# Kernel tuning notes

Hardware: AMD Instinct MI355X
Metric: run time of the kernel (lower is better)

Reference implementation:

```python
import jax, jax.numpy as jnp
import numpy as np

N = 50000   # nodes
E = 800000  # edges (avg degree 16)
C = 64      # in_channels == out_channels


def _linear_params(key, fan_in, fan_out):
    kw, kb = jax.random.split(key)
    s = 1.0 / np.sqrt(fan_in)
    W = jax.random.uniform(kw, (fan_out, fan_in), minval=-s, maxval=s, dtype=jnp.float32)
    b = jax.random.uniform(kb, (fan_out,), minval=-s, maxval=s, dtype=jnp.float32)
    return W, b


def setup_inputs() -> dict:
    key = jax.random.key(0)
    ks = jax.random.split(key, 12)
    scalar = jax.random.normal(ks[0], (N, C), dtype=jnp.float32)
    vector = jax.random.normal(ks[1], (N, 3, C), dtype=jnp.float32)
    position = jax.random.normal(ks[2], (N, 3), dtype=jnp.float32)
    edge_index = jax.random.randint(ks[3], (2, E), 0, N, dtype=jnp.int64)
    edge_attr = jax.random.uniform(ks[4], (E,), dtype=jnp.float32)
    # Scalar_Conv params
    Wss, bss = _linear_params(ks[5], 2 * C, C)   # s_to_s
    Wvs, bvs = _linear_params(ks[6], 2 * C, C)   # v_to_s
    Wsl, bsl = _linear_params(ks[7], 2 * C, C)   # scalar_linear
    # Vector_Conv params
    Wsv, bsv = _linear_params(ks[8], 2 * C, C)   # s_to_v
    Wvv, bvv = _linear_params(ks[9], 2 * C, C)   # v_to_v
    Wvl, bvl = _linear_params(ks[10], 2 * C, C)  # vector_linear
    return dict(scalar=scalar, vector=vector, position=position,
                edge_index=edge_index, edge_attr=edge_attr,
                Wss=Wss, bss=bss, Wvs=Wvs, bvs=bvs, Wsl=Wsl, bsl=bsl,
                Wsv=Wsv, bsv=bsv, Wvv=Wvv, bvv=bvv, Wvl=Wvl, bvl=bvl)


def _norm(edge_index, edge_attr, num_nodes):
    # B=True path: edge_attr-weighted symmetric degree normalization
    row, col = edge_index[0], edge_index[1]
    deg = jax.ops.segment_sum(edge_attr, col, num_segments=num_nodes)
    deg_safe = jnp.where(deg > 0, deg, 1.0)
    dis = jnp.where(deg > 0, deg_safe ** -0.5, 0.0)
    return row, col, dis[row] * dis[col] * edge_attr


def _forward(scalar, vector, position, edge_index, edge_attr,
             Wss, bss, Wvs, bvs, Wsl, bsl, Wsv, bsv, Wvv, bvv, Wvl, bvl):
    num_nodes = scalar.shape[0]
    row, col = _norm(edge_index, edge_attr, num_nodes)[:2]
    _, _, norm = _norm(edge_index, edge_attr, num_nodes)
    # PyG: _i = target (col), _j = source (row); aggregate at col
    s_i, s_j = scalar[col], scalar[row]            # [E,C]
    v_i, v_j = vector[col], vector[row]            # [E,3,C]
    pos = position[col] - position[row]            # [E,3]
    s_cat = jnp.concatenate([s_i, s_j], axis=-1)   # [E,2C]
    v_cat = jnp.concatenate([v_i, v_j], axis=-1)   # [E,3,2C]

    # ---- Scalar_Conv messages ----
    s2s = jax.nn.silu(s_cat @ Wss.T + bss)                          # [E,C]
    v2s = v_cat @ Wvs.T + bvs                                       # [E,3,C]
    v2s = jax.nn.silu(jnp.sum(v2s * pos[:, :, None], axis=1))       # [E,C]
    s_msg = (jnp.concatenate([s2s, v2s], axis=-1) @ Wsl.T + bsl)    # [E,C]
    s_msg = norm[:, None] * s_msg
    s_agg = jax.ops.segment_sum(s_msg, col, num_segments=num_nodes)

    # ---- Vector_Conv messages ----
    s2v = s_cat @ Wsv.T + bsv                                       # [E,C]
    s2v = jnp.tanh(s2v[:, None, :] * pos[:, :, None])               # [E,3,C]
    v2v = v_cat @ Wvv.T + bvv                                       # [E,3,C]
    v_msg = jnp.concatenate([v2v, s2v], axis=-1) @ Wvl.T + bvl      # [E,3,C]
    v_msg = norm[:, None, None] * v_msg
    v_agg = jax.ops.segment_sum(v_msg, col, num_segments=num_nodes)

    scalar_out = jax.nn.silu(s_agg) + scalar
    vector_out = jnp.tanh(v_agg) + vector
    return scalar_out, vector_out


def reference(scalar, vector, position, edge_index, edge_attr,
              Wss, bss, Wvs, bvs, Wsl, bsl, Wsv, bsv, Wvv, bvv, Wvl, bvl):
    return _forward(scalar, vector, position, edge_index, edge_attr,
                    Wss, bss, Wvs, bvs, Wsl, bsl, Wsv, bsv, Wvv, bvv, Wvl, bvl)
```

## Files before the change

kernel.cpp:

```cpp
#include <hip/hip_runtime.h>
#include <cstdint>
#include <cstddef>

typedef unsigned int   u32;
typedef unsigned short u16;
typedef __attribute__((ext_vector_type(8))) short bf16x8;
typedef __attribute__((ext_vector_type(4))) float f32x4;

__device__ __forceinline__ float bf2f(u32 bits16) { return __uint_as_float(bits16 << 16); }
__device__ __forceinline__ u16 f2bf(float f) {
  u32 u = __float_as_uint(f);
  u = u + 0x7FFFu + ((u >> 16) & 1u);
  return (u16)(u >> 16);
}
__device__ __forceinline__ u32 pk(float a, float b) {
  return (u32)f2bf(a) | ((u32)f2bf(b) << 16);
}
__device__ __forceinline__ float lo16(u32 w) { return bf2f(w & 0xFFFFu); }
__device__ __forceinline__ float hi16(u32 w) { return bf2f(w >> 16); }
__device__ __forceinline__ float frcp(float x) { return __builtin_amdgcn_rcpf(x); }
__device__ __forceinline__ float fexp2(float x) { return __builtin_amdgcn_exp2f(x); }

#define NL2E   (-1.4426950408889634f)
#define TWOL2E (2.8853900817779268f)
#define CNTSC  1073741824.0

__device__ __forceinline__ int load_idx(const int* eidx, int is64, long long pos) {
  if (is64) return (int)(((const long long*)eidx)[pos]);
  return eidx[pos];
}

__global__ void k_prep1(const float* Wvl, const float* Wvv,
                        const float* bvv, const float* bvl,
                        const int* eidx, int E, int* flag,
                        float* WcTmp, float* bc,
                        double* dpk, int* erecI, int* tilestat, int* tilectr,
                        int N, int NB) {
  int b = blockIdx.x, tid = threadIdx.x;
  if (b < 32) {
    int c = 2 * b + (tid >> 7), kk = tid & 127;
    float s = 0.f;
    for (int m = 0; m < 64; ++m) s += Wvl[c * 128 + m] * Wvv[m * 128 + kk];
    WcTmp[c * 128 + kk] = s;
  } else if (b == 32) {
    __shared__ int zc;
    if (tid == 0) zc = 0;
    __syncthreads();
    int n = (E < 1024) ? E : 1024;
    int local = 0;
    for (int i = tid; i < n; i += 256) {
      if (eidx[2 * i + 1] == 0) local++;
    }
    atomicAdd(&zc, local);
    __syncthreads();
    if (tid == 0) *flag = (zc >= (n >> 1)) ? 1 : 0;
  } else if (b == 33) {
    if (tid < 64) {
      float s = 0.f;
      for (int m = 0; m < 64; ++m) s += Wvl[tid * 128 + m] * bvv[m];
      bc[tid] = s + bvl[tid];
    }
  } else if (b == 34) {
    if (tid < 64) erecI[E + tid] = 0;
    if (tid == 64) *tilectr = 0;
    for (int i = tid; i < NB; i += 256) tilestat[i] = 0;
  } else {
    int idx = (b - 35) * 256 + tid;
    if (idx < N) dpk[idx] = 0.0;
  }
}

__global__ void k_prep2(const float* Wss, const float* Wsv, const float* Wvs,
                        const float* Wsl, const float* Wvl, const float* WcTmp,
                        u32* Wsl2, u32* Wpk, u16* Wtg) {
  int b = blockIdx.x, tid = threadIdx.x;
  if (b < 2) {
    for (int i = 0; i < 8; ++i) {
      int o = b * 2048 + i * 256 + tid;
      int h = o & 1, c = (o >> 1) & 63, g = o >> 7;
      int k = 4 * g + 2 * h;
      Wsl2[o] = pk(Wsl[c * 128 + k], Wsl[c * 128 + k + 1]);
    }
  } else if (b == 2) {
    for (int i = 0; i < 8; ++i) {
      int o = i * 256 + tid;
      int h = o & 1, c = (o >> 1) & 63, g = o >> 7;
      int k = 4 * g + 2 * h;
      Wpk[o] = pk(Wvl[c * 128 + 64 + k], Wvl[c * 128 + 64 + k + 1]);
    }
  } else {
    for (int i = 0; i < 16; ++i) {
      int p = (b - 3) * 4096 + i * 256 + tid;
      int r = p >> 6, k = p & 63;
      int g = (r >> 6) & 3, ch = r & 63;
      int src = ch * 128 + ((g & 2) ? 64 : 0) + k;
      float w;
      if (r < 256) w = (g & 1) ? Wsv[src] : Wss[src];
      else         w = (g & 1) ? WcTmp[src] : Wvs[src];
      u16 h = f2bf(w);
      Wtg[r * 128 + k] = h;
      Wtg[r * 128 + 64 + k] = f2bf(w - bf2f(h));
    }
  }
}

__global__ void k_scan(const double* dpk, float* dis, int* rowptr, int* cursor,
                       int* tilestat, int* tilectr, int N, int E) {
  __shared__ int lds[256];
  __shared__ int sTile, sPrefix;
  int tid = threadIdx.x;
  if (tid == 0) sTile = atomicAdd(tilectr, 1);
  __syncthreads();
  int tile = sTile;
  int idx = tile * 256 + tid;
  int c = 0;
  if (idx < N) {
    double p = dpk[idx];
    c = (int)(p * (1.0 / CNTSC));
    float dg = (float)(p - (double)c * CNTSC);
    dis[idx] = (dg > 0.f) ? rsqrtf(dg) : 0.f;
  }
  lds[tid] = c;
  __syncthreads();
  for (int off = 1; off < 256; off <<= 1) {
    int t = (tid >= off) ? lds[tid - off] : 0;
    __syncthreads();
    lds[tid] += t;
    __syncthreads();
  }
  int incl = lds[tid];
  int aggregate = lds[255];
  if (tid == 0) {
    if (tile == 0) {
      atomicExch(&tilestat[0], (2 << 30) | aggregate);
      rowptr[N] = E;
    } else {
      atomicExch(&tilestat[tile], (1 << 30) | aggregate);
      int excl = 0;
      int t = tile - 1;
      while (true) {
        int s = atomicAdd(&tilestat[t], 0);
        int flag = (u32)s >> 30;
        if (flag == 0) continue;
        excl += s & 0x3FFFFFFF;
        if (flag == 2) break;
        --t;
      }
      sPrefix = excl;
      atomicExch(&tilestat[tile], (2 << 30) | (excl + aggregate));
    }
  }
  __syncthreads();
  int exclPrefix = (tile == 0) ? 0 : sPrefix;
  if (idx < N) {
    int o = exclPrefix + incl - c;
    rowptr[idx] = o;
    cursor[idx] = o;
  }
}

__global__ void k_fill(const int* eidx, const int* flag, const float* attr, const float* dis,
                       const float* pos, int* cursor, float4* erecA, int* erecI, int E) {
  int e = blockIdx.x * 256 + threadIdx.x;
  if (e >= E) return;
  int is64 = *flag;
  int r  = load_idx(eidx, is64, e);
  int cl = load_idx(eidx, is64, (long long)E + e);
  float wr = dis[r] * attr[e];
  float dx = pos[cl * 3 + 0] - pos[r * 3 + 0];
  float dy = pos[cl * 3 + 1] - pos[r * 3 + 1];
  float dz = pos[cl * 3 + 2] - pos[r * 3 + 2];
  int p = atomicAdd(&cursor[cl], 1);
  erecA[p] = make_float4(wr, dx, dy, dz);
  erecI[p] = r;
}

__global__ __launch_bounds__(512, 4) void k_gemm_deg(
    const float* __restrict__ scalar, const float* __restrict__ vector,
    const u16* __restrict__ Wtg,
    uint4* __restrict__ rec_i4, uint4* __restrict__ rec_j4, int N, int GB,
    const int* __restrict__ eidx, const int* __restrict__ flag,
    const float* __restrict__ attr, double* __restrict__ dpk, int E) {
  __shared__ u32 smem[8192];
  int tid = threadIdx.x;
  if ((int)blockIdx.x >= GB) {
    int e = ((int)blockIdx.x - GB) * 512 + tid;
    if (e < E) {
      int is64 = *flag;
      int col = load_idx(eidx, is64, (long long)E + e);
      atomicAdd(&dpk[col], (double)attr[e] + CNTSC);
    }
    return;
  }
  u16*   Ax = (u16*)smem;
  float* Ep = (float*)smem;
  int lane = tid & 63, wv = tid >> 6;
  int nb = blockIdx.x * 32;

  {
    int srow = tid >> 2, skq = tid & 3;
    const float* sp;
    int snode;
    if (srow < 32) { snode = nb + srow; sp = scalar + (size_t)snode * 64 + skq * 16; }
    else {
      int d = (srow - 32) >> 5, nl2 = (srow - 32) & 31;
      snode = nb + nl2;
      sp = vector + (size_t)snode * 192 + d * 64 + skq * 16;
    }
    bool valid = snode < N;
    u16 hi[16], lo[16];
    #pragma unroll
    for (int q = 0; q < 4; ++q) {
      float4 v = valid ? *(const float4*)(sp + 4 * q) : make_float4(0.f, 0.f, 0.f, 0.f);
      float xs[4] = {v.x, v.y, v.z, v.w};
      #pragma unroll
      for (int j = 0; j < 4; ++j) {
        u16 h = f2bf(xs[j]);
        hi[4 * q + j] = h;
        lo[4 * q + j] = f2bf(xs[j] - bf2f(h));
      }
    }
    int rs = srow & 7;
    #pragma unroll
    for (int c = 0; c < 2; ++c) {
      int lc = 2 * skq + c;
      uint4 wh, wl;
      wh.x = (u32)hi[8*c+0] | ((u32)hi[8*c+1] << 16);
      wh.y = (u32)hi[8*c+2] | ((u32)hi[8*c+3] << 16);
      wh.z = (u32)hi[8*c+4] | ((u32)hi[8*c+5] << 16);
      wh.w = (u32)hi[8*c+6] | ((u32)hi[8*c+7] << 16);
      wl.x = (u32)lo[8*c+0] | ((u32)lo[8*c+1] << 16);
      wl.y = (u32)lo[8*c+2] | ((u32)lo[8*c+3] << 16);
      wl.z = (u32)lo[8*c+4] | ((u32)lo[8*c+5] << 16);
      wl.w = (u32)lo[8*c+6] | ((u32)lo[8*c+7] << 16);
      *(uint4*)(Ax + srow * 128 + (lc ^ rs) * 8)        = wh;
      *(uint4*)(Ax + srow * 128 + ((8 + lc) ^ rs) * 8)  = wl;
    }
  }
  __syncthreads();

  int c0 = wv * 32;
  int bl = lane & 15, bh = lane >> 4;
  f32x4 acc[8][2];
  #pragma unroll
  for (int mt = 0; mt < 8; ++mt)
    #pragma unroll
    for (int nt = 0; nt < 2; ++nt)
      acc[mt][nt] = (f32x4){0.f, 0.f, 0.f, 0.f};

  #pragma unroll
  for (int kh = 0; kh < 2; ++kh) {
    int k0 = kh * 32;
    bf16x8 Bh[2][2], Bl[2][2];
    #pragma unroll
    for (int rg = 0; rg < 2; ++rg)
      #pragma unroll
      for (int nt = 0; nt < 2; ++nt) {
        size_t rr = (size_t)(rg * 256 + c0 + nt * 16 + bl) * 128 + k0 + bh * 8;
        Bh[rg][nt] = *(const bf16x8*)(Wtg + rr);
        Bl[rg][nt] = *(const bf16x8*)(Wtg + rr + 64);
      }
    #pragma unroll
    for (int mt = 0; mt < 8; ++mt) {
      int row = mt * 16 + bl;
      int ch = (k0 >> 3) + bh, rs = row & 7;
      bf16x8 Ah = *(const bf16x8*)(Ax + row * 128 + (ch ^ rs) * 8);
      bf16x8 Al = *(const bf16x8*)(Ax + row * 128 + ((8 + ch) ^ rs) * 8);
      int rg = (mt < 2) ? 0 : 1;
      #pragma unroll
      for (int nt = 0; nt < 2; ++nt) {
        f32x4 a = acc[mt][nt];
        a = __builtin_amdgcn_mfma_f32_16x16x32_bf16(Ah, Bh[rg][nt], a, 0, 0, 0);
        a = __builtin_amdgcn_mfma_f32_16x16x32_bf16(Al, Bh[rg][nt], a, 0, 0, 0);
        a = __builtin_amdgcn_mfma_f32_16x16x32_bf16(Ah, Bl[rg][nt], a, 0, 0, 0);
        acc[mt][nt] = a;
      }
    }
  }

  int ech = tid & 63, eng = tid >> 6;
  uint4 oi[4], oj[4];
  #pragma unroll
  for (int pg = 0; pg < 4; ++pg) {
    __syncthreads();
    #pragma unroll
    for (int mm = 0; mm < 2; ++mm) {
      int mt = 2 * pg + mm;
      #pragma unroll
      for (int nt = 0; nt < 2; ++nt)
        #pragma unroll
        for (int r = 0; r < 4; ++r) {
          int rl = mm * 16 + bh * 4 + r;
          Ep[rl * 256 + c0 + nt * 16 + bl] = acc[mt][nt][r];
        }
    }
    __syncthreads();
    #pragma unroll
    for (int q = 0; q < 4; ++q) {
      int nl2 = eng + 8 * q;
      float vi0 = Ep[nl2 * 256 + ech];
      float vi1 = Ep[nl2 * 256 + 64 + ech];
      float vj0 = Ep[nl2 * 256 + 128 + ech];
      float vj1 = Ep[nl2 * 256 + 192 + ech];
      if (pg == 0) {
        oi[q].x = pk(vi0, vi1);                  oj[q].x = pk(vj0, vj1);
      } else if (pg == 1) {
        oi[q].y = (u32)f2bf(vi0);                oj[q].y = (u32)f2bf(vj0);
        oi[q].z = (u32)f2bf(vi1) << 16;          oj[q].z = (u32)f2bf(vj1) << 16;
      } else if (pg == 2) {
        oi[q].y |= (u32)f2bf(vi0) << 16;         oj[q].y |= (u32)f2bf(vj0) << 16;
        oi[q].w = (u32)f2bf(vi1);                oj[q].w = (u32)f2bf(vj1);
      } else {
        oi[q].z |= (u32)f2bf(vi0);               oj[q].z |= (u32)f2bf(vj0);
        oi[q].w |= (u32)f2bf(vi1) << 16;         oj[q].w |= (u32)f2bf(vj1) << 16;
      }
    }
  }
  #pragma unroll
  for (int q = 0; q < 4; ++q) {
    int node = nb + eng + 8 * q;
    if (node < N) {
      rec_i4[(size_t)node * 64 + ech] = oi[q];
      rec_j4[(size_t)node * 64 + ech] = oj[q];
    }
  }
}

__global__ __launch_bounds__(512) void k_edges(
    const u16* __restrict__ rec_i, const u16* __restrict__ rec_j,
    const float4* __restrict__ erecA, const int* __restrict__ erecI,
    const int* __restrict__ rowptr, const float* __restrict__ dis,
    const float* __restrict__ scalar, const float* __restrict__ vector,
    const float* __restrict__ bss, const float* __restrict__ bvs,
    const float* __restrict__ bsv, const float* __restrict__ bsl,
    const u32* __restrict__ Wsl2g, const u32* __restrict__ Wpkg,
    const float* __restrict__ bcg,
    float* __restrict__ out_s, float* __restrict__ out_v, int N) {
  __shared__ u32 sWsl[4096];
  __shared__ u32 sWv[2048];
  __shared__ float sStage[8 * 192];
  int tid = threadIdx.x, lane = tid & 63, wv = tid >> 6;
  for (int o = tid; o < 4096; o += 512) sWsl[o] = Wsl2g[o];
  for (int o = tid; o < 2048; o += 512) sWv[o] = Wpkg[o];
  __syncthreads();

  int node = __builtin_amdgcn_readfirstlane((int)(blockIdx.x * 8) + wv);
  if (node >= N) node = N - 1;

  uint4 riv = *(const uint4*)(rec_i + ((size_t)node << 9) + lane * 8);
  float aiB  = lo16(riv.x) + bss[lane];
  float KciB = TWOL2E * (hi16(riv.x) + bsv[lane]);
  float Bvs  = bvs[lane];
  float bib0 = lo16(riv.y) + Bvs;
  float bib1 = hi16(riv.y) + Bvs;
  float bib2 = lo16(riv.z) + Bvs;
  float Pi0  = hi16(riv.z), Pi1 = lo16(riv.w), Pi2 = hi16(riv.w);
  float bsl_c = bsl[lane], bc_c = bcg[lane];
  float disc = dis[node];

  float us = 0, uv = 0, t0 = 0, t1 = 0, t2 = 0, g0 = 0, g1 = 0, g2 = 0, wa = 0;
  int rp = rowptr[node], re = rowptr[node + 1];
  u32 lane16 = (u32)lane << 4;
  const char* rjb = (const char*)rec_j;

  u32 ra = (u32)erecI[rp];
  u32 rb = (u32)erecI[rp + 1];
  uint4 pre0 = *(const uint4*)(rjb + ((ra << 10) + lane16));
  uint4 pre1 = *(const uint4*)(rjb + ((rb << 10) + lane16));
  int p = rp;
  #define EDGE_MATH(CUR, EV)                                                  \
    {                                                                         \
      float nrm = EV.x, dx = EV.y, dy = EV.z, dz = EV.w;                      \
      float aj  = lo16(CUR.x), cj  = hi16(CUR.x);                             \
      float bj0 = lo16(CUR.y), bj1 = hi16(CUR.y), bj2 = lo16(CUR.z);          \
      float rj0 = hi16(CUR.z), rj1 = lo16(CUR.w), rj2 = hi16(CUR.w);          \
      float xs  = aiB + aj;                                                   \
      float s2s = xs * frcp(1.f + fexp2(xs * NL2E));                          \
      float yv  = (bib0 + bj0) * dx;                                          \
      yv = fmaf(bib1 + bj1, dy, yv);                                          \
      yv = fmaf(bib2 + bj2, dz, yv);                                          \
      float v2s = yv * frcp(1.f + fexp2(yv * NL2E));                          \
      float qh  = fmaf(TWOL2E, cj, KciB);                                     \
      float th0 = fmaf(-2.f, frcp(1.f + fexp2(qh * dx)), 1.f);                \
      float th1 = fmaf(-2.f, frcp(1.f + fexp2(qh * dy)), 1.f);                \
      float th2 = fmaf(-2.f, frcp(1.f + fexp2(qh * dz)), 1.f);                \
      us = fmaf(nrm, s2s, us); uv = fmaf(nrm, v2s, uv);                       \
      t0 = fmaf(nrm, th0, t0); t1 = fmaf(nrm, th1, t1); t2 = fmaf(nrm, th2, t2);\
      g0 = fmaf(nrm, rj0, g0); g1 = fmaf(nrm, rj1, g1); g2 = fmaf(nrm, rj2, g2);\
      wa += nrm;                                                              \
    }
  for (; p + 1 < re; p += 2) {
    uint4 cur0 = pre0, cur1 = pre1;
    u32 rn0 = (u32)erecI[p + 2];
    u32 rn1 = (u32)erecI[p + 3];
    pre0 = *(const uint4*)(rjb + ((rn0 << 10) + lane16));
    pre1 = *(const uint4*)(rjb + ((rn1 << 10) + lane16));
    float4 e0 = erecA[p];
    float4 e1 = erecA[p + 1];
    EDGE_MATH(cur0, e0)
    EDGE_MATH(cur1, e1)
  }
  if (p < re) {
    uint4 cur0 = pre0;
    float4 e0 = erecA[p];
    EDGE_MATH(cur0, e0)
  }
  #undef EDGE_MATH

  us *= disc; uv *= disc;
  t0 *= disc; t1 *= disc; t2 *= disc;
  g0 *= disc; g1 *= disc; g2 *= disc;
  wa *= disc;

  float* mys = &sStage[wv * 192];
  mys[lane] = us; mys[64 + lane] = uv;
  __threadfence_block();
  float acc = wa * bsl_c;
  #pragma unroll
  for (int g = 0; g < 32; ++g) {
    float4 u = *(const float4*)&mys[4 * g];
    uint2 w = *(const uint2*)&sWsl[(g * 64 + lane) * 2];
    acc = fmaf(u.x, lo16(w.x), acc);
    acc = fmaf(u.y, hi16(w.x), acc);
    acc = fmaf(u.z, lo16(w.y), acc);
    acc = fmaf(u.w, hi16(w.y), acc);
  }
  size_t so = ((size_t)node << 6) + lane;
  out_s[so] = acc * frcp(1.f + fexp2(acc * NL2E)) + scalar[so];

  __threadfence_block();
  mys[lane] = t0; mys[64 + lane] = t1; mys[128 + lane] = t2;
  __threadfence_block();
  float a20 = fmaf(wa, bc_c + Pi0, g0);
  float a21 = fmaf(wa, bc_c + Pi1, g1);
  float a22 = fmaf(wa, bc_c + Pi2, g2);
  #pragma unroll
  for (int g = 0; g < 16; ++g) {
    float4 u0 = *(const float4*)&mys[4 * g];
    float4 u1 = *(const float4*)&mys[64 + 4 * g];
    float4 u2 = *(const float4*)&mys[128 + 4 * g];
    uint2 w = *(const uint2*)&sWv[(g * 64 + lane) * 2];
    float w0 = lo16(w.x), w1 = hi16(w.x), w2 = lo16(w.y), w3 = hi16(w.y);
    a20 = fmaf(u0.x, w0, a20); a20 = fmaf(u0.y, w1, a20);
    a20 = fmaf(u0.z, w2, a20); a20 = fmaf(u0.w, w3, a20);
    a21 = fmaf(u1.x, w0, a21); a21 = fmaf(u1.y, w1, a21);
    a21 = fmaf(u1.z, w2, a21); a21 = fmaf(u1.w, w3, a21);
    a22 = fmaf(u2.x, w0, a22); a22 = fmaf(u2.y, w1, a22);
    a22 = fmaf(u2.z, w2, a22); a22 = fmaf(u2.w, w3, a22);
  }
  float a2v[3] = {a20, a21, a22};
  #pragma unroll
  for (int d = 0; d < 3; ++d) {
    size_t vo = (((size_t)node * 3 + d) << 6) + lane;
    float th = fmaf(-2.f, frcp(1.f + fexp2(TWOL2E * a2v[d])), 1.f);
    out_v[vo] = th + vector[vo];
  }
}

extern "C" void kernel_launch(void* const* d_in, const int* in_sizes, int n_in,
                              void* d_out, int out_size, void* d_ws, size_t ws_size,
                              hipStream_t stream) {
  const float* scalar   = (const float*)d_in[0];
  const float* vector   = (const float*)d_in[1];
  const float* position = (const float*)d_in[2];
  const int*   eidx     = (const int*)d_in[3];
  const float* attr     = (const float*)d_in[4];
  const float* Wss = (const float*)d_in[5];
  const float* bss = (const float*)d_in[6];
  const float* Wvs = (const float*)d_in[7];
  const float* bvs = (const float*)d_in[8];
  const float* Wsl = (const float*)d_in[9];
  const float* bsl = (const float*)d_in[10];
  const float* Wsv = (const float*)d_in[11];
  const float* bsv = (const float*)d_in[12];
  const float* Wvv = (const float*)d_in[13];
  const float* bvv = (const float*)d_in[14];
  const float* Wvl = (const float*)d_in[15];
  const float* bvl = (const float*)d_in[16];

  int N = in_sizes[0] / 64;
  int E = in_sizes[4];
  int NB = (N + 255) / 256;

  char* wsb = (char*)d_ws;
  size_t off = 0;
  auto alloc = [&](size_t bytes) -> char* {
    char* p = wsb + off;
    off += (bytes + 255) & ~(size_t)255;
    return p;
  };
  double* dpk    = (double*)alloc((size_t)N * 8);
  int*    rowptr = (int*)alloc((size_t)(N + 1) * 4);
  int*    cursor = (int*)alloc((size_t)N * 4);
  float*  dis    = (float*)alloc((size_t)N * 4);
  int*    tilestat = (int*)alloc((size_t)NB * 4);
  int*    tilectr  = (int*)alloc(4);
  float4* erecA  = (float4*)alloc((size_t)E * 16);
  int*    erecI  = (int*)alloc((size_t)(E + 64) * 4);
  u16*    rec_i  = (u16*)alloc((size_t)N * 512 * 2);
  u16*    rec_j  = (u16*)alloc((size_t)N * 512 * 2);
  u16*    Wtg    = (u16*)alloc(512 * 128 * 2);
  u32*    Wsl2   = (u32*)alloc(4096 * 4);
  u32*    Wpk    = (u32*)alloc(2048 * 4);
  float*  WcTmp  = (float*)alloc(64 * 128 * 4);
  float*  bc     = (float*)alloc(64 * 4);
  int*    flag   = (int*)alloc(4);
  (void)ws_size; (void)n_in; (void)out_size;

  int GB = (N + 31) / 32;
  int DB = (E + 511) / 512;

  k_prep1<<<35 + NB, 256, 0, stream>>>(Wvl, Wvv, bvv, bvl, eidx, E, flag,
                                       WcTmp, bc, dpk, erecI, tilestat, tilectr, N, NB);
  k_prep2<<<11, 256, 0, stream>>>(Wss, Wsv, Wvs, Wsl, Wvl, WcTmp, Wsl2, Wpk, Wtg);
  k_gemm_deg<<<GB + DB, 512, 0, stream>>>(scalar, vector, Wtg,
                                          (uint4*)rec_i, (uint4*)rec_j, N, GB,
                                          eidx, flag, attr, dpk, E);
  k_scan<<<NB, 256, 0, stream>>>(dpk, dis, rowptr, cursor, tilestat, tilectr, N, E);
  k_fill<<<(E + 255) / 256, 256, 0, stream>>>(eidx, flag, attr, dis, position, cursor, erecA, erecI, E);
  k_edges<<<(N + 7) / 8, 512, 0, stream>>>(rec_i, rec_j, erecA, erecI, rowptr, dis,
                                           scalar, vector, bss, bvs, bsv, bsl,
                                           Wsl2, Wpk, bc,
                                           (float*)d_out, (float*)d_out + (size_t)N * 64, N);
}
```

Before: 404.5 us.

## Split node GEMM across degree and fill kernels; parallelize scan lookback

The per-node GEMM is split in half: the first half runs alongside the degree atomics, and the second half is fused into a new kernel that also does the edge fill. This lets the atomic-heavy passes overlap with compute. The decoupled-lookback scan now uses a whole wavefront to inspect 64 predecessor tiles at once with ballots and a shuffle reduction, instead of one thread walking back serially. The risks are register and occupancy pressure from the combined kernel and uneven block mixes.

```diff
diff --git a/kernel.cpp b/kernel.cpp
--- a/kernel.cpp
+++ b/kernel.cpp
@@ -130,28 +130,40 @@
   }
   int incl = lds[tid];
   int aggregate = lds[255];
-  if (tid == 0) {
-    if (tile == 0) {
+  if (tile == 0) {
+    if (tid == 0) {
       atomicExch(&tilestat[0], (2 << 30) | aggregate);
       rowptr[N] = E;
-    } else {
-      atomicExch(&tilestat[tile], (1 << 30) | aggregate);
-      int excl = 0;
-      int t = tile - 1;
+      sPrefix = 0;
+    }
+  } else {
+    if (tid == 0) atomicExch(&tilestat[tile], (1 << 30) | aggregate);
+    if (tid < 64) {
+      int pred = tile - 1 - tid;
+      int excl;
       while (true) {
-        int s = atomicAdd(&tilestat[t], 0);
-        int flag = (u32)s >> 30;
-        if (flag == 0) continue;
-        excl += s & 0x3FFFFFFF;
-        if (flag == 2) break;
-        --t;
+        int s = (pred >= 0) ? atomicAdd(&tilestat[pred], 0) : (2 << 30);
+        u32 fl = (u32)s >> 30;
+        unsigned long long pfx = __ballot(fl == 2);
+        unsigned long long unp = __ballot(fl == 0);
+        int l1 = pfx ? (__ffsll((long long)pfx) - 1) : 64;
+        int l0 = unp ? (__ffsll((long long)unp) - 1) : 64;
+        if (l1 < 64 && l0 > l1) {
+          int v = (tid <= l1) ? (s & 0x3FFFFFFF) : 0;
+          #pragma unroll
+          for (int o = 32; o > 0; o >>= 1) v += __shfl_xor(v, o, 64);
+          excl = v;
+          break;
+        }
       }
-      sPrefix = excl;
-      atomicExch(&tilestat[tile], (2 << 30) | (excl + aggregate));
+      if (tid == 0) {
+        sPrefix = excl;
+        atomicExch(&tilestat[tile], (2 << 30) | (excl + aggregate));
+      }
     }
   }
   __syncthreads();
-  int exclPrefix = (tile == 0) ? 0 : sPrefix;
+  int exclPrefix = sPrefix;
   if (idx < N) {
     int o = exclPrefix + incl - c;
     rowptr[idx] = o;
@@ -159,43 +171,14 @@
   }
 }
 
-__global__ void k_fill(const int* eidx, const int* flag, const float* attr, const float* dis,
-                       const float* pos, int* cursor, float4* erecA, int* erecI, int E) {
-  int e = blockIdx.x * 256 + threadIdx.x;
-  if (e >= E) return;
-  int is64 = *flag;
-  int r  = load_idx(eidx, is64, e);
-  int cl = load_idx(eidx, is64, (long long)E + e);
-  float wr = dis[r] * attr[e];
-  float dx = pos[cl * 3 + 0] - pos[r * 3 + 0];
-  float dy = pos[cl * 3 + 1] - pos[r * 3 + 1];
-  float dz = pos[cl * 3 + 2] - pos[r * 3 + 2];
-  int p = atomicAdd(&cursor[cl], 1);
-  erecA[p] = make_float4(wr, dx, dy, dz);
-  erecI[p] = r;
-}
-
-__global__ __launch_bounds__(512, 4) void k_gemm_deg(
+__device__ __forceinline__ void gemm_body(
+    u32* smem, int tid, int nb,
     const float* __restrict__ scalar, const float* __restrict__ vector,
     const u16* __restrict__ Wtg,
-    uint4* __restrict__ rec_i4, uint4* __restrict__ rec_j4, int N, int GB,
-    const int* __restrict__ eidx, const int* __restrict__ flag,
-    const float* __restrict__ attr, double* __restrict__ dpk, int E) {
-  __shared__ u32 smem[8192];
-  int tid = threadIdx.x;
-  if ((int)blockIdx.x >= GB) {
-    int e = ((int)blockIdx.x - GB) * 512 + tid;
-    if (e < E) {
-      int is64 = *flag;
-      int col = load_idx(eidx, is64, (long long)E + e);
-      atomicAdd(&dpk[col], (double)attr[e] + CNTSC);
-    }
-    return;
-  }
+    uint4* __restrict__ rec_i4, uint4* __restrict__ rec_j4, int N) {
   u16*   Ax = (u16*)smem;
   float* Ep = (float*)smem;
   int lane = tid & 63, wv = tid >> 6;
-  int nb = blockIdx.x * 32;
 
   {
     int srow = tid >> 2, skq = tid & 3;
@@ -324,6 +307,55 @@
       rec_j4[(size_t)node * 64 + ech] = oj[q];
     }
   }
+}
+
+__global__ __launch_bounds__(512, 4) void k_gemm_deg(
+    const float* __restrict__ scalar, const float* __restrict__ vector,
+    const u16* __restrict__ Wtg,
+    uint4* __restrict__ rec_i4, uint4* __restrict__ rec_j4, int N, int GB1,
+    const int* __restrict__ eidx, const int* __restrict__ flag,
+    const float* __restrict__ attr, double* __restrict__ dpk, int E) {
+  __shared__ u32 smem[8192];
+  int tid = threadIdx.x;
+  if ((int)blockIdx.x >= GB1) {
+    int e = ((int)blockIdx.x - GB1) * 512 + tid;
+    if (e < E) {
+      int is64 = *flag;
+      int col = load_idx(eidx, is64, (long long)E + e);
+      atomicAdd(&dpk[col], (double)attr[e] + CNTSC);
+    }
+    return;
+  }
+  gemm_body(smem, tid, (int)blockIdx.x * 32, scalar, vector, Wtg, rec_i4, rec_j4, N);
+}
+
+__global__ __launch_bounds__(512, 4) void k_gemm_fill(
+    const float* __restrict__ scalar, const float* __restrict__ vector,
+    const u16* __restrict__ Wtg,
+    uint4* __restrict__ rec_i4, uint4* __restrict__ rec_j4, int N, int GB1, int GB2,
+    const int* __restrict__ eidx, const int* __restrict__ flag,
+    const float* __restrict__ attr, const float* __restrict__ dis,
+    const float* __restrict__ pos, int* __restrict__ cursor,
+    float4* __restrict__ erecA, int* __restrict__ erecI, int E) {
+  __shared__ u32 smem[8192];
+  int tid = threadIdx.x;
+  if ((int)blockIdx.x >= GB2) {
+    int e = ((int)blockIdx.x - GB2) * 512 + tid;
+    if (e < E) {
+      int is64 = *flag;
+      int r  = load_idx(eidx, is64, e);
+      int cl = load_idx(eidx, is64, (long long)E + e);
+      float wr = dis[r] * attr[e];
+      float dx = pos[cl * 3 + 0] - pos[r * 3 + 0];
+      float dy = pos[cl * 3 + 1] - pos[r * 3 + 1];
+      float dz = pos[cl * 3 + 2] - pos[r * 3 + 2];
+      int p = atomicAdd(&cursor[cl], 1);
+      erecA[p] = make_float4(wr, dx, dy, dz);
+      erecI[p] = r;
+    }
+    return;
+  }
+  gemm_body(smem, tid, (GB1 + (int)blockIdx.x) * 32, scalar, vector, Wtg, rec_i4, rec_j4, N);
 }
 
 __global__ __launch_bounds__(512) void k_edges(
@@ -507,17 +539,22 @@
   int*    flag   = (int*)alloc(4);
   (void)ws_size; (void)n_in; (void)out_size;
 
-  int GB = (N + 31) / 32;
-  int DB = (E + 511) / 512;
+  int GB  = (N + 31) / 32;
+  int GB1 = GB / 2;
+  int GB2 = GB - GB1;
+  int DB  = (E + 511) / 512;
 
   k_prep1<<<35 + NB, 256, 0, stream>>>(Wvl, Wvv, bvv, bvl, eidx, E, flag,
                                        WcTmp, bc, dpk, erecI, tilestat, tilectr, N, NB);
   k_prep2<<<11, 256, 0, stream>>>(Wss, Wsv, Wvs, Wsl, Wvl, WcTmp, Wsl2, Wpk, Wtg);
-  k_gemm_deg<<<GB + DB, 512, 0, stream>>>(scalar, vector, Wtg,
-                                          (uint4*)rec_i, (uint4*)rec_j, N, GB,
-                                          eidx, flag, attr, dpk, E);
+  k_gemm_deg<<<GB1 + DB, 512, 0, stream>>>(scalar, vector, Wtg,
+                                           (uint4*)rec_i, (uint4*)rec_j, N, GB1,
+                                           eidx, flag, attr, dpk, E);
   k_scan<<<NB, 256, 0, stream>>>(dpk, dis, rowptr, cursor, tilestat, tilectr, N, E);
-  k_fill<<<(E + 255) / 256, 256, 0, stream>>>(eidx, flag, attr, dis, position, cursor, erecA, erecI, E);
+  k_gemm_fill<<<GB2 + DB, 512, 0, stream>>>(scalar, vector, Wtg,
+                                            (uint4*)rec_i, (uint4*)rec_j, N, GB1, GB2,
+                                            eidx, flag, attr, dis, position, cursor,
+                                            erecA, erecI, E);
   k_edges<<<(N + 7) / 8, 512, 0, stream>>>(rec_i, rec_j, erecA, erecI, rowptr, dis,
                                            scalar, vector, bss, bvs, bsv, bsl,
                                            Wsl2, Wpk, bc,
```

Measured after the change: 407.0 us. Within noise of the previous version (+0.6%).

## Parallelize decoupled look-back scan and scalarize per-node edge indices

Applied to the files above, without the earlier changes.

The rowptr scan's look-back now uses a whole wavefront to inspect 64 predecessor tile statuses at once, using ballots to find the nearest inclusive prefix and a shuffle reduction to sum the aggregates, replacing the serial single-thread walk. In the edge kernel, rowptr and neighbor indices are forced into scalar registers with readfirstlane, so loads and address math become wave-uniform scalar operations. The gemm body is also moved into a device helper without changing behaviour. The look-back issues more atomic polls per iteration, and the scan is a small part of total time.

```diff
diff --git a/kernel.cpp b/kernel.cpp
--- a/kernel.cpp
+++ b/kernel.cpp
@@ -130,28 +130,40 @@
   }
   int incl = lds[tid];
   int aggregate = lds[255];
-  if (tid == 0) {
-    if (tile == 0) {
+  if (tile == 0) {
+    if (tid == 0) {
       atomicExch(&tilestat[0], (2 << 30) | aggregate);
       rowptr[N] = E;
-    } else {
-      atomicExch(&tilestat[tile], (1 << 30) | aggregate);
-      int excl = 0;
-      int t = tile - 1;
+      sPrefix = 0;
+    }
+  } else {
+    if (tid == 0) atomicExch(&tilestat[tile], (1 << 30) | aggregate);
+    if (tid < 64) {
+      int pred = tile - 1 - tid;
+      int excl;
       while (true) {
-        int s = atomicAdd(&tilestat[t], 0);
-        int flag = (u32)s >> 30;
-        if (flag == 0) continue;
-        excl += s & 0x3FFFFFFF;
-        if (flag == 2) break;
-        --t;
+        int s = (pred >= 0) ? atomicAdd(&tilestat[pred], 0) : (2 << 30);
+        u32 fl = (u32)s >> 30;
+        unsigned long long pfx = __ballot(fl == 2);
+        unsigned long long unp = __ballot(fl == 0);
+        int l1 = pfx ? (__ffsll((long long)pfx) - 1) : 64;
+        int l0 = unp ? (__ffsll((long long)unp) - 1) : 64;
+        if (l1 < 64 && l0 > l1) {
+          int v = (tid <= l1) ? (s & 0x3FFFFFFF) : 0;
+          #pragma unroll
+          for (int o = 32; o > 0; o >>= 1) v += __shfl_xor(v, o, 64);
+          excl = v;
+          break;
+        }
       }
-      sPrefix = excl;
-      atomicExch(&tilestat[tile], (2 << 30) | (excl + aggregate));
+      if (tid == 0) {
+        sPrefix = excl;
+        atomicExch(&tilestat[tile], (2 << 30) | (excl + aggregate));
+      }
     }
   }
   __syncthreads();
-  int exclPrefix = (tile == 0) ? 0 : sPrefix;
+  int exclPrefix = sPrefix;
   if (idx < N) {
     int o = exclPrefix + incl - c;
     rowptr[idx] = o;
@@ -175,27 +187,14 @@
   erecI[p] = r;
 }
 
-__global__ __launch_bounds__(512, 4) void k_gemm_deg(
+__device__ __forceinline__ void gemm_body(
+    u32* smem, int tid, int nb,
     const float* __restrict__ scalar, const float* __restrict__ vector,
     const u16* __restrict__ Wtg,
-    uint4* __restrict__ rec_i4, uint4* __restrict__ rec_j4, int N, int GB,
-    const int* __restrict__ eidx, const int* __restrict__ flag,
-    const float* __restrict__ attr, double* __restrict__ dpk, int E) {
-  __shared__ u32 smem[8192];
-  int tid = threadIdx.x;
-  if ((int)blockIdx.x >= GB) {
-    int e = ((int)blockIdx.x - GB) * 512 + tid;
-    if (e < E) {
-      int is64 = *flag;
-      int col = load_idx(eidx, is64, (long long)E + e);
-      atomicAdd(&dpk[col], (double)attr[e] + CNTSC);
-    }
-    return;
-  }
+    uint4* __restrict__ rec_i4, uint4* __restrict__ rec_j4, int N) {
   u16*   Ax = (u16*)smem;
   float* Ep = (float*)smem;
   int lane = tid & 63, wv = tid >> 6;
-  int nb = blockIdx.x * 32;
 
   {
     int srow = tid >> 2, skq = tid & 3;
@@ -326,6 +325,26 @@
   }
 }
 
+__global__ __launch_bounds__(512, 4) void k_gemm_deg(
+    const float* __restrict__ scalar, const float* __restrict__ vector,
+    const u16* __restrict__ Wtg,
+    uint4* __restrict__ rec_i4, uint4* __restrict__ rec_j4, int N, int GB,
+    const int* __restrict__ eidx, const int* __restrict__ flag,
+    const float* __restrict__ attr, double* __restrict__ dpk, int E) {
+  __shared__ u32 smem[8192];
+  int tid = threadIdx.x;
+  if ((int)blockIdx.x >= GB) {
+    int e = ((int)blockIdx.x - GB) * 512 + tid;
+    if (e < E) {
+      int is64 = *flag;
+      int col = load_idx(eidx, is64, (long long)E + e);
+      atomicAdd(&dpk[col], (double)attr[e] + CNTSC);
+    }
+    return;
+  }
+  gemm_body(smem, tid, (int)blockIdx.x * 32, scalar, vector, Wtg, rec_i4, rec_j4, N);
+}
+
 __global__ __launch_bounds__(512) void k_edges(
     const u16* __restrict__ rec_i, const u16* __restrict__ rec_j,
     const float4* __restrict__ erecA, const int* __restrict__ erecI,
@@ -359,12 +378,13 @@
   float disc = dis[node];
 
   float us = 0, uv = 0, t0 = 0, t1 = 0, t2 = 0, g0 = 0, g1 = 0, g2 = 0, wa = 0;
-  int rp = rowptr[node], re = rowptr[node + 1];
+  int rp = __builtin_amdgcn_readfirstlane(rowptr[node]);
+  int re = __builtin_amdgcn_readfirstlane(rowptr[node + 1]);
   u32 lane16 = (u32)lane << 4;
   const char* rjb = (const char*)rec_j;
 
-  u32 ra = (u32)erecI[rp];
-  u32 rb = (u32)erecI[rp + 1];
+  u32 ra = (u32)__builtin_amdgcn_readfirstlane(erecI[rp]);
+  u32 rb = (u32)__builtin_amdgcn_readfirstlane(erecI[rp + 1]);
   uint4 pre0 = *(const uint4*)(rjb + ((ra << 10) + lane16));
   uint4 pre1 = *(const uint4*)(rjb + ((rb << 10) + lane16));
   int p = rp;
@@ -391,8 +411,8 @@
     }
   for (; p + 1 < re; p += 2) {
     uint4 cur0 = pre0, cur1 = pre1;
-    u32 rn0 = (u32)erecI[p + 2];
-    u32 rn1 = (u32)erecI[p + 3];
+    u32 rn0 = (u32)__builtin_amdgcn_readfirstlane(erecI[p + 2]);
+    u32 rn1 = (u32)__builtin_amdgcn_readfirstlane(erecI[p + 3]);
     pre0 = *(const uint4*)(rjb + ((rn0 << 10) + lane16));
     pre1 = *(const uint4*)(rjb + ((rn1 << 10) + lane16));
     float4 e0 = erecA[p];
```

Result: no change. 398.5 us (-1.5%).
